# Performance work log

Measured on AMD Instinct MI355X. Metric: run time of the kernel, lower is better.

The kernel has to match this reference:

```python
import jax, jax.numpy as jnp
import numpy as np

N = 50000
K = 4
D_IN = 256
D_OUT = 64
E = 800000

def setup_inputs() -> dict:
    key = jax.random.key(0)
    k1, k2, k3, k4, k5 = jax.random.split(key, 5)
    x = jax.random.normal(k1, (N, K, D_IN), dtype=jnp.float32)
    weight = jax.random.normal(k2, (D_IN, D_OUT), dtype=jnp.float32) * (1.0 / np.sqrt(D_IN))
    adj_rows = jax.random.randint(k3, (E,), 0, N, dtype=jnp.int32)
    adj_cols = jax.random.randint(k4, (E,), 0, N, dtype=jnp.int32)
    adj_vals = jax.random.uniform(k5, (E,), dtype=jnp.float32)
    return {"x": x, "weight": weight, "adj_rows": adj_rows, "adj_cols": adj_cols, "adj_vals": adj_vals}

def reference(x, weight, adj_rows, adj_cols, adj_vals):
    # x: [N, K, D_in]; weight: [D_in, D_out]
    # dropout p=0.0 / eval mode -> identity
    # support = x @ W for every sample k, vectorized over K
    support = jnp.einsum('nkd,df->nkf', x, weight)          # [N, K, D_out]
    # sparse adj matmul: out[r] += vals[e] * support[cols[e]]
    msgs = adj_vals[:, None, None] * support[adj_cols]       # [E, K, D_out]
    out = jax.ops.segment_sum(msgs, adj_rows, num_segments=N)  # [N, K, D_out]
    return jax.nn.relu(out)
```

## Files before the change

kernel.cpp:

```cpp
#include <hip/hip_runtime.h>
#include <hip/hip_bf16.h>
#include <stdint.h>

#define D_IN   256
#define D_OUT  64
#define KHEADS 4
#define ROWLEN 256
#define GBM    128
#define LDAB   72
#define LDWB   72
#define CAP    128

typedef __attribute__((ext_vector_type(8))) short bf16x8;
typedef __attribute__((ext_vector_type(4))) float f32x4;

__device__ __forceinline__ unsigned short f2bf(float f) {
  unsigned u = __float_as_uint(f);
  return (unsigned short)((u + 0x7fffu + ((u >> 16) & 1u)) >> 16);
}

__global__ __launch_bounds__(256) void gemm_mfma(const float* __restrict__ X,
                                                 const float* __restrict__ W,
                                                 signed char* __restrict__ Sq,
                                                 float* __restrict__ scaleArr,
                                                 int M, int Nnodes) {
  __shared__ unsigned short lA[GBM * LDAB];
  __shared__ unsigned short lWt[64 * LDWB];
  const int t    = threadIdx.x;
  const int wave = t >> 6;
  const int lane = t & 63;
  const int q    = lane >> 4;
  const int l16  = lane & 15;
  const long row0 = (long)blockIdx.x * GBM;

  f32x4 acc[2][4];
#pragma unroll
  for (int rb = 0; rb < 2; ++rb)
#pragma unroll
    for (int cb = 0; cb < 4; ++cb) acc[rb][cb] = (f32x4){0.f, 0.f, 0.f, 0.f};

  for (int k0 = 0; k0 < D_IN; k0 += 64) {
#pragma unroll
    for (int j = 0; j < 8; ++j) {
      int flat = t + j * 256;
      int r    = flat >> 4;
      int kk   = (flat & 15) << 2;
      long gr  = row0 + r;
      if (gr >= M) gr = M - 1;
      float4 v = *(const float4*)&X[gr * D_IN + k0 + kk];
      ushort4 o;
      o.x = f2bf(v.x); o.y = f2bf(v.y); o.z = f2bf(v.z); o.w = f2bf(v.w);
      *(ushort4*)&lA[r * LDAB + kk] = o;
    }
#pragma unroll
    for (int j = 0; j < 4; ++j) {
      int flat = t + j * 256;
      int kr   = flat >> 4;
      int nn   = (flat & 15) << 2;
      float4 v = *(const float4*)&W[(size_t)(k0 + kr) * D_OUT + nn];
      lWt[(nn + 0) * LDWB + kr] = f2bf(v.x);
      lWt[(nn + 1) * LDWB + kr] = f2bf(v.y);
      lWt[(nn + 2) * LDWB + kr] = f2bf(v.z);
      lWt[(nn + 3) * LDWB + kr] = f2bf(v.w);
    }
    __syncthreads();

#pragma unroll
    for (int s = 0; s < 2; ++s) {
      bf16x8 a0 = *(const bf16x8*)&lA[(wave * 32 + 0  + l16) * LDAB + s * 32 + q * 8];
      bf16x8 a1 = *(const bf16x8*)&lA[(wave * 32 + 16 + l16) * LDAB + s * 32 + q * 8];
#pragma unroll
      for (int cb = 0; cb < 4; ++cb) {
        bf16x8 b = *(const bf16x8*)&lWt[(cb * 16 + l16) * LDWB + s * 32 + q * 8];
        acc[0][cb] = __builtin_amdgcn_mfma_f32_16x16x32_bf16(a0, b, acc[0][cb], 0, 0, 0);
        acc[1][cb] = __builtin_amdgcn_mfma_f32_16x16x32_bf16(a1, b, acc[1][cb], 0, 0, 0);
      }
    }
    __syncthreads();
  }

  float nm0 = 0.f, nm1 = 0.f;
#pragma unroll
  for (int cb = 0; cb < 4; ++cb)
#pragma unroll
    for (int reg = 0; reg < 4; ++reg) {
      nm0 = fmaxf(nm0, fabsf(acc[0][cb][reg]));
      nm1 = fmaxf(nm1, fabsf(acc[1][cb][reg]));
    }
#pragma unroll
  for (int d = 1; d < 16; d <<= 1) {
    nm0 = fmaxf(nm0, __shfl_xor(nm0, d, 64));
    nm1 = fmaxf(nm1, __shfl_xor(nm1, d, 64));
  }
  const float inv0 = (nm0 > 0.f) ? 127.f / nm0 : 0.f;
  const float inv1 = (nm1 > 0.f) ? 127.f / nm1 : 0.f;
  const int node_base = blockIdx.x * 32 + wave * 8;
  if (l16 == 0) {
    int n0 = node_base + q;
    int n1 = node_base + 4 + q;
    if (n0 < Nnodes) scaleArr[n0] = nm0 / 127.f;
    if (n1 < Nnodes) scaleArr[n1] = nm1 / 127.f;
  }
#pragma unroll
  for (int rb = 0; rb < 2; ++rb) {
    const float inv = rb ? inv1 : inv0;
#pragma unroll
    for (int cb = 0; cb < 4; ++cb)
#pragma unroll
      for (int reg = 0; reg < 4; ++reg) {
        long r = row0 + wave * 32 + rb * 16 + q * 4 + reg;
        if (r < M) {
          int qi = (int)rintf(acc[rb][cb][reg] * inv);
          Sq[r * D_OUT + cb * 16 + l16] = (signed char)qi;
        }
      }
  }
}

__global__ __launch_bounds__(256) void place_kernel(const int* __restrict__ rows,
                                                    const int* __restrict__ cols,
                                                    const float* __restrict__ vals,
                                                    const float* __restrict__ scaleArr,
                                                    int* __restrict__ cnt,
                                                    uint2* __restrict__ ecv, int E) {
  int e = blockIdx.x * 256 + threadIdx.x;
  if (e < E) {
    int r = rows[e];
    int c = cols[e];
    float vp = vals[e] * scaleArr[c];
    int pos = atomicAdd(&cnt[r], 1);
    if (pos < CAP)
      ecv[((size_t)r << 7) + pos] = make_uint2((unsigned)c, __float_as_uint(vp));
  }
}

__global__ __launch_bounds__(256) void gather_kernel(const int* __restrict__ Sqi,
                                                     const int* __restrict__ cnt,
                                                     const uint2* __restrict__ ecv,
                                                     float* __restrict__ out, int n) {
  const int lane = threadIdx.x & 63;
  const int r = blockIdx.x * 4 + (threadIdx.x >> 6);
  if (r >= n) return;
  int deg = cnt[r];
  if (deg > CAP) deg = CAP;
  const uint2* __restrict__ bucket = ecv + ((size_t)r << 7);

  float4 a0 = make_float4(0.f, 0.f, 0.f, 0.f);
  float4 a1 = a0, a2 = a0, a3 = a0;
  int i = 0;
  for (; i + 4 <= deg; i += 4) {
    uint2 c0 = bucket[i], c1 = bucket[i + 1], c2 = bucket[i + 2], c3 = bucket[i + 3];
    int w0 = Sqi[(size_t)c0.x * 64 + lane];
    int w1 = Sqi[(size_t)c1.x * 64 + lane];
    int w2 = Sqi[(size_t)c2.x * 64 + lane];
    int w3 = Sqi[(size_t)c3.x * 64 + lane];
    float v0 = __uint_as_float(c0.y), v1 = __uint_as_float(c1.y);
    float v2 = __uint_as_float(c2.y), v3 = __uint_as_float(c3.y);
    a0.x += v0 * (float)(w0 << 24 >> 24); a0.y += v0 * (float)(w0 << 16 >> 24);
    a0.z += v0 * (float)(w0 <<  8 >> 24); a0.w += v0 * (float)(w0 >> 24);
    a1.x += v1 * (float)(w1 << 24 >> 24); a1.y += v1 * (float)(w1 << 16 >> 24);
    a1.z += v1 * (float)(w1 <<  8 >> 24); a1.w += v1 * (float)(w1 >> 24);
    a2.x += v2 * (float)(w2 << 24 >> 24); a2.y += v2 * (float)(w2 << 16 >> 24);
    a2.z += v2 * (float)(w2 <<  8 >> 24); a2.w += v2 * (float)(w2 >> 24);
    a3.x += v3 * (float)(w3 << 24 >> 24); a3.y += v3 * (float)(w3 << 16 >> 24);
    a3.z += v3 * (float)(w3 <<  8 >> 24); a3.w += v3 * (float)(w3 >> 24);
  }
  for (; i < deg; ++i) {
    uint2 c0 = bucket[i];
    int w0 = Sqi[(size_t)c0.x * 64 + lane];
    float v0 = __uint_as_float(c0.y);
    a0.x += v0 * (float)(w0 << 24 >> 24); a0.y += v0 * (float)(w0 << 16 >> 24);
    a0.z += v0 * (float)(w0 <<  8 >> 24); a0.w += v0 * (float)(w0 >> 24);
  }
  float4 res;
  res.x = fmaxf(a0.x + a1.x + a2.x + a3.x, 0.f);
  res.y = fmaxf(a0.y + a1.y + a2.y + a3.y, 0.f);
  res.z = fmaxf(a0.z + a1.z + a2.z + a3.z, 0.f);
  res.w = fmaxf(a0.w + a1.w + a2.w + a3.w, 0.f);
  *(float4*)&out[(size_t)r * ROWLEN + (lane << 2)] = res;
}

extern "C" void kernel_launch(void* const* d_in, const int* in_sizes, int n_in,
                              void* d_out, int out_size, void* d_ws, size_t ws_size,
                              hipStream_t stream) {
  const float* x    = (const float*)d_in[0];
  const float* w    = (const float*)d_in[1];
  const int*   rows = (const int*)d_in[2];
  const int*   cols = (const int*)d_in[3];
  const float* vals = (const float*)d_in[4];
  float* out = (float*)d_out;

  const int E = in_sizes[2];
  const int N = in_sizes[0] / (KHEADS * D_IN);
  const int M = N * KHEADS;

  char* ws = (char*)d_ws;
  size_t o = 0;
  signed char* Sq = (signed char*)(ws + o); o += (size_t)M * D_OUT;
  o = (o + 15) & ~(size_t)15;
  float* scaleArr = (float*)(ws + o); o += (size_t)N * sizeof(float);
  o = (o + 15) & ~(size_t)15;
  int* cnt = (int*)(ws + o); o += (size_t)N * sizeof(int);
  o = (o + 15) & ~(size_t)15;
  uint2* ecv = (uint2*)(ws + o);

  hipMemsetAsync(cnt, 0, (size_t)N * sizeof(int), stream);

  gemm_mfma<<<(M + GBM - 1) / GBM, 256, 0, stream>>>(x, w, Sq, scaleArr, M, N);
  place_kernel<<<(E + 255) / 256, 256, 0, stream>>>(rows, cols, vals, scaleArr, cnt, ecv, E);
  gather_kernel<<<(N + 3) / 4, 256, 0, stream>>>((const int*)Sq, cnt, ecv, out, N);
}
```

Before: 395.6 us.

## Fuse GEMM and edge placement into one launch, load A directly to registers

The GEMM and the edge-bucketing kernels become one launch whose blocks are interleaved: one GEMM block for every two placement blocks. To allow this, the per-node scale is no longer folded into edge values at placement time; the gather kernel now reads scaleArr per edge instead. The GEMM now loads W fully into LDS once and streams X straight from global memory into registers with software prefetch, removing the A-tile LDS staging and the per-k barriers. The gather loop drops its scalar tail by clamping indices and zeroing weights, and the output is written with nontemporal stores. The trade-off is an extra scale gather per edge in the gather phase and a 33KB LDS footprint that placement blocks also carry.

Result: faster. 376.2 us (-4.9%).

```diff
diff --git a/kernel.cpp b/kernel.cpp
--- a/kernel.cpp
+++ b/kernel.cpp
@@ -1,5 +1,4 @@
 #include <hip/hip_runtime.h>
-#include <hip/hip_bf16.h>
 #include <stdint.h>
 
 #define D_IN   256
@@ -7,8 +6,7 @@
 #define KHEADS 4
 #define ROWLEN 256
 #define GBM    128
-#define LDAB   72
-#define LDWB   72
+#define LDW    264
 #define CAP    128
 
 typedef __attribute__((ext_vector_type(8))) short bf16x8;
@@ -19,19 +17,45 @@
   return (unsigned short)((u + 0x7fffu + ((u >> 16) & 1u)) >> 16);
 }
 
-__global__ __launch_bounds__(256) void gemm_mfma(const float* __restrict__ X,
-                                                 const float* __restrict__ W,
-                                                 signed char* __restrict__ Sq,
-                                                 float* __restrict__ scaleArr,
-                                                 int M, int Nnodes) {
-  __shared__ unsigned short lA[GBM * LDAB];
-  __shared__ unsigned short lWt[64 * LDWB];
+__device__ __forceinline__ bf16x8 pack8(float4 a, float4 b) {
+  bf16x8 r;
+  r[0] = (short)f2bf(a.x); r[1] = (short)f2bf(a.y);
+  r[2] = (short)f2bf(a.z); r[3] = (short)f2bf(a.w);
+  r[4] = (short)f2bf(b.x); r[5] = (short)f2bf(b.y);
+  r[6] = (short)f2bf(b.z); r[7] = (short)f2bf(b.w);
+  return r;
+}
+
+__device__ __forceinline__ void gemm_body(const float* __restrict__ X,
+                                          const float* __restrict__ W,
+                                          signed char* __restrict__ Sq,
+                                          float* __restrict__ scaleArr,
+                                          int M, int Nnodes, int gb) {
+  __shared__ unsigned short lWt[64 * LDW];
   const int t    = threadIdx.x;
   const int wave = t >> 6;
   const int lane = t & 63;
   const int q    = lane >> 4;
   const int l16  = lane & 15;
-  const long row0 = (long)blockIdx.x * GBM;
+  const long row0 = (long)gb * GBM;
+
+#pragma unroll
+  for (int j = 0; j < 16; ++j) {
+    int flat = t + j * 256;
+    int kr   = flat >> 4;
+    int nn   = (flat & 15) << 2;
+    float4 v = *(const float4*)&W[(size_t)kr * D_OUT + nn];
+    lWt[(nn + 0) * LDW + kr] = f2bf(v.x);
+    lWt[(nn + 1) * LDW + kr] = f2bf(v.y);
+    lWt[(nn + 2) * LDW + kr] = f2bf(v.z);
+    lWt[(nn + 3) * LDW + kr] = f2bf(v.w);
+  }
+  __syncthreads();
+
+  long r0 = row0 + wave * 32 + l16;       if (r0 > (long)M - 1) r0 = M - 1;
+  long r1 = row0 + wave * 32 + 16 + l16;  if (r1 > (long)M - 1) r1 = M - 1;
+  const float* __restrict__ x0 = X + r0 * D_IN + q * 8;
+  const float* __restrict__ x1 = X + r1 * D_IN + q * 8;
 
   f32x4 acc[2][4];
 #pragma unroll
@@ -39,44 +63,29 @@
 #pragma unroll
     for (int cb = 0; cb < 4; ++cb) acc[rb][cb] = (f32x4){0.f, 0.f, 0.f, 0.f};
 
-  for (int k0 = 0; k0 < D_IN; k0 += 64) {
-#pragma unroll
-    for (int j = 0; j < 8; ++j) {
-      int flat = t + j * 256;
-      int r    = flat >> 4;
-      int kk   = (flat & 15) << 2;
-      long gr  = row0 + r;
-      if (gr >= M) gr = M - 1;
-      float4 v = *(const float4*)&X[gr * D_IN + k0 + kk];
-      ushort4 o;
-      o.x = f2bf(v.x); o.y = f2bf(v.y); o.z = f2bf(v.z); o.w = f2bf(v.w);
-      *(ushort4*)&lA[r * LDAB + kk] = o;
+  float4 c00 = *(const float4*)(x0);
+  float4 c01 = *(const float4*)(x0 + 4);
+  float4 c10 = *(const float4*)(x1);
+  float4 c11 = *(const float4*)(x1 + 4);
+#pragma unroll
+  for (int s = 0; s < 8; ++s) {
+    float4 n00, n01, n10, n11;
+    if (s < 7) {
+      const float* p0 = x0 + (s + 1) * 32;
+      const float* p1 = x1 + (s + 1) * 32;
+      n00 = *(const float4*)(p0); n01 = *(const float4*)(p0 + 4);
+      n10 = *(const float4*)(p1); n11 = *(const float4*)(p1 + 4);
     }
-#pragma unroll
-    for (int j = 0; j < 4; ++j) {
-      int flat = t + j * 256;
-      int kr   = flat >> 4;
-      int nn   = (flat & 15) << 2;
-      float4 v = *(const float4*)&W[(size_t)(k0 + kr) * D_OUT + nn];
-      lWt[(nn + 0) * LDWB + kr] = f2bf(v.x);
-      lWt[(nn + 1) * LDWB + kr] = f2bf(v.y);
-      lWt[(nn + 2) * LDWB + kr] = f2bf(v.z);
-      lWt[(nn + 3) * LDWB + kr] = f2bf(v.w);
+    bf16x8 a0 = pack8(c00, c01);
+    bf16x8 a1 = pack8(c10, c11);
+    const unsigned short* wb = &lWt[l16 * LDW + s * 32 + q * 8];
+#pragma unroll
+    for (int cb = 0; cb < 4; ++cb) {
+      bf16x8 b = *(const bf16x8*)(wb + cb * 16 * LDW);
+      acc[0][cb] = __builtin_amdgcn_mfma_f32_16x16x32_bf16(a0, b, acc[0][cb], 0, 0, 0);
+      acc[1][cb] = __builtin_amdgcn_mfma_f32_16x16x32_bf16(a1, b, acc[1][cb], 0, 0, 0);
     }
-    __syncthreads();
-
-#pragma unroll
-    for (int s = 0; s < 2; ++s) {
-      bf16x8 a0 = *(const bf16x8*)&lA[(wave * 32 + 0  + l16) * LDAB + s * 32 + q * 8];
-      bf16x8 a1 = *(const bf16x8*)&lA[(wave * 32 + 16 + l16) * LDAB + s * 32 + q * 8];
-#pragma unroll
-      for (int cb = 0; cb < 4; ++cb) {
-        bf16x8 b = *(const bf16x8*)&lWt[(cb * 16 + l16) * LDWB + s * 32 + q * 8];
-        acc[0][cb] = __builtin_amdgcn_mfma_f32_16x16x32_bf16(a0, b, acc[0][cb], 0, 0, 0);
-        acc[1][cb] = __builtin_amdgcn_mfma_f32_16x16x32_bf16(a1, b, acc[1][cb], 0, 0, 0);
-      }
-    }
-    __syncthreads();
+    if (s < 7) { c00 = n00; c01 = n01; c10 = n10; c11 = n11; }
   }
 
   float nm0 = 0.f, nm1 = 0.f;
@@ -94,7 +103,7 @@
   }
   const float inv0 = (nm0 > 0.f) ? 127.f / nm0 : 0.f;
   const float inv1 = (nm1 > 0.f) ? 127.f / nm1 : 0.f;
-  const int node_base = blockIdx.x * 32 + wave * 8;
+  const int node_base = gb * 32 + wave * 8;
   if (l16 == 0) {
     int n0 = node_base + q;
     int n1 = node_base + 4 + q;
@@ -117,24 +126,40 @@
   }
 }
 
-__global__ __launch_bounds__(256) void place_kernel(const int* __restrict__ rows,
-                                                    const int* __restrict__ cols,
-                                                    const float* __restrict__ vals,
-                                                    const float* __restrict__ scaleArr,
-                                                    int* __restrict__ cnt,
-                                                    uint2* __restrict__ ecv, int E) {
-  int e = blockIdx.x * 256 + threadIdx.x;
+__device__ __forceinline__ void place_body(const int* __restrict__ rows,
+                                           const int* __restrict__ cols,
+                                           const float* __restrict__ vals,
+                                           int* __restrict__ cnt,
+                                           uint2* __restrict__ ecv, int E, int pb) {
+  int e = pb * 256 + threadIdx.x;
   if (e < E) {
     int r = rows[e];
     int c = cols[e];
-    float vp = vals[e] * scaleArr[c];
+    float v = vals[e];
     int pos = atomicAdd(&cnt[r], 1);
     if (pos < CAP)
-      ecv[((size_t)r << 7) + pos] = make_uint2((unsigned)c, __float_as_uint(vp));
+      ecv[((size_t)r << 7) + pos] = make_uint2((unsigned)c, __float_as_uint(v));
+  }
+}
+
+__global__ __launch_bounds__(256) void fused_phase1(
+    const float* __restrict__ X, const float* __restrict__ W,
+    signed char* __restrict__ Sq, float* __restrict__ scaleArr,
+    const int* __restrict__ rows, const int* __restrict__ cols,
+    const float* __restrict__ vals, int* __restrict__ cnt,
+    uint2* __restrict__ ecv, int M, int Nnodes, int E, int G, int P) {
+  const int bid = blockIdx.x;
+  const int g = bid / 3, r3 = bid - 3 * g;
+  if (r3 == 0) {
+    if (g < G) gemm_body(X, W, Sq, scaleArr, M, Nnodes, g);
+  } else {
+    int pb = 2 * g + r3 - 1;
+    if (pb < P) place_body(rows, cols, vals, cnt, ecv, E, pb);
   }
 }
 
 __global__ __launch_bounds__(256) void gather_kernel(const int* __restrict__ Sqi,
+                                                     const float* __restrict__ scaleArr,
                                                      const int* __restrict__ cnt,
                                                      const uint2* __restrict__ ecv,
                                                      float* __restrict__ out, int n) {
@@ -147,15 +172,21 @@
 
   float4 a0 = make_float4(0.f, 0.f, 0.f, 0.f);
   float4 a1 = a0, a2 = a0, a3 = a0;
-  int i = 0;
-  for (; i + 4 <= deg; i += 4) {
-    uint2 c0 = bucket[i], c1 = bucket[i + 1], c2 = bucket[i + 2], c3 = bucket[i + 3];
+  for (int i = 0; i < deg; i += 4) {
+    int i1 = (i + 1 < deg) ? i + 1 : deg - 1;
+    int i2 = (i + 2 < deg) ? i + 2 : deg - 1;
+    int i3 = (i + 3 < deg) ? i + 3 : deg - 1;
+    uint2 c0 = bucket[i], c1 = bucket[i1], c2 = bucket[i2], c3 = bucket[i3];
+    float s0 = scaleArr[c0.x], s1 = scaleArr[c1.x];
+    float s2 = scaleArr[c2.x], s3 = scaleArr[c3.x];
     int w0 = Sqi[(size_t)c0.x * 64 + lane];
     int w1 = Sqi[(size_t)c1.x * 64 + lane];
     int w2 = Sqi[(size_t)c2.x * 64 + lane];
     int w3 = Sqi[(size_t)c3.x * 64 + lane];
-    float v0 = __uint_as_float(c0.y), v1 = __uint_as_float(c1.y);
-    float v2 = __uint_as_float(c2.y), v3 = __uint_as_float(c3.y);
+    float v0 = __uint_as_float(c0.y) * s0;
+    float v1 = (i + 1 < deg) ? __uint_as_float(c1.y) * s1 : 0.f;
+    float v2 = (i + 2 < deg) ? __uint_as_float(c2.y) * s2 : 0.f;
+    float v3 = (i + 3 < deg) ? __uint_as_float(c3.y) * s3 : 0.f;
     a0.x += v0 * (float)(w0 << 24 >> 24); a0.y += v0 * (float)(w0 << 16 >> 24);
     a0.z += v0 * (float)(w0 <<  8 >> 24); a0.w += v0 * (float)(w0 >> 24);
     a1.x += v1 * (float)(w1 << 24 >> 24); a1.y += v1 * (float)(w1 << 16 >> 24);
@@ -165,19 +196,12 @@
     a3.x += v3 * (float)(w3 << 24 >> 24); a3.y += v3 * (float)(w3 << 16 >> 24);
     a3.z += v3 * (float)(w3 <<  8 >> 24); a3.w += v3 * (float)(w3 >> 24);
   }
-  for (; i < deg; ++i) {
-    uint2 c0 = bucket[i];
-    int w0 = Sqi[(size_t)c0.x * 64 + lane];
-    float v0 = __uint_as_float(c0.y);
-    a0.x += v0 * (float)(w0 << 24 >> 24); a0.y += v0 * (float)(w0 << 16 >> 24);
-    a0.z += v0 * (float)(w0 <<  8 >> 24); a0.w += v0 * (float)(w0 >> 24);
-  }
-  float4 res;
-  res.x = fmaxf(a0.x + a1.x + a2.x + a3.x, 0.f);
-  res.y = fmaxf(a0.y + a1.y + a2.y + a3.y, 0.f);
-  res.z = fmaxf(a0.z + a1.z + a2.z + a3.z, 0.f);
-  res.w = fmaxf(a0.w + a1.w + a2.w + a3.w, 0.f);
-  *(float4*)&out[(size_t)r * ROWLEN + (lane << 2)] = res;
+  f32x4 res;
+  res[0] = fmaxf(a0.x + a1.x + a2.x + a3.x, 0.f);
+  res[1] = fmaxf(a0.y + a1.y + a2.y + a3.y, 0.f);
+  res[2] = fmaxf(a0.z + a1.z + a2.z + a3.z, 0.f);
+  res[3] = fmaxf(a0.w + a1.w + a2.w + a3.w, 0.f);
+  __builtin_nontemporal_store(res, (f32x4*)&out[(size_t)r * ROWLEN + (lane << 2)]);
 }
 
 extern "C" void kernel_launch(void* const* d_in, const int* in_sizes, int n_in,
@@ -206,7 +230,9 @@
 
   hipMemsetAsync(cnt, 0, (size_t)N * sizeof(int), stream);
 
-  gemm_mfma<<<(M + GBM - 1) / GBM, 256, 0, stream>>>(x, w, Sq, scaleArr, M, N);
-  place_kernel<<<(E + 255) / 256, 256, 0, stream>>>(rows, cols, vals, scaleArr, cnt, ecv, E);
-  gather_kernel<<<(N + 3) / 4, 256, 0, stream>>>((const int*)Sq, cnt, ecv, out, N);
-}
+  const int G = (M + GBM - 1) / GBM;
+  const int P = (E + 255) / 256;
+  fused_phase1<<<3 * G, 256, 0, stream>>>(x, w, Sq, scaleArr, rows, cols, vals,
+                                          cnt, ecv, M, N, E, G, P);
+  gather_kernel<<<(N + 3) / 4, 256, 0, stream>>>((const int*)Sq, scaleArr, cnt, ecv, out, N);
+}
```
